# Kernel optimization log

Measured on AMD Instinct MI355X. Metric: run time of the kernel, lower is better.

Reference implementation:

```python
import jax, jax.numpy as jnp
import numpy as np

B, L, D_MODEL, HEADS = 4, 2048, 1024, 16
D_K = D_MODEL // HEADS
EPS = 1e-8
ROPE_BASE = 10000.0


def setup_inputs() -> dict:
    key = jax.random.key(0)
    k1, k2, k3 = jax.random.split(key, 3)
    x = jax.random.normal(k1, (B, L, D_MODEL), jnp.float32)
    W_in = jax.random.normal(k2, (3 * D_MODEL, D_MODEL), jnp.float32) * 0.02
    W_o = jax.random.normal(k3, (D_MODEL, D_MODEL), jnp.float32) * 0.02
    return {"x": x, "W_in": W_in, "W_o": W_o}


def _layer_norm(x, eps=EPS):
    # F.layer_norm with no affine params
    mu = jnp.mean(x, axis=-1, keepdims=True)
    var = jnp.var(x, axis=-1, keepdims=True)
    return (x - mu) * jax.lax.rsqrt(var + eps)


def _rope(x):
    # x: [B, H, L, d_k]; interleaved-pair rotary embedding
    seq = x.shape[2]
    half = x.shape[-1] // 2
    inv_freq = 1.0 / (ROPE_BASE ** (jnp.arange(half, dtype=jnp.float32) * 2.0 / x.shape[-1]))
    ang = jnp.arange(seq, dtype=jnp.float32)[:, None] * inv_freq[None, :]  # [L, half]
    cos, sin = jnp.cos(ang), jnp.sin(ang)
    x1, x2 = x[..., 0::2], x[..., 1::2]
    r1 = x1 * cos - x2 * sin
    r2 = x1 * sin + x2 * cos
    return jnp.stack([r1, r2], axis=-1).reshape(x.shape)


def reference(x, W_in, W_o):
    h = _layer_norm(x)
    qkv = h @ W_in.T  # [B, L, 3*D]
    q, k, v = jnp.split(qkv, 3, axis=-1)
    to_heads = lambda t: t.reshape(B, L, HEADS, D_K).transpose(0, 2, 1, 3)  # [B,H,L,dk]
    q, k, v = to_heads(q), to_heads(k), to_heads(v)
    q, k = _rope(q), _rope(k)
    scale = 1.0 / np.sqrt(D_K).astype(np.float32)
    scores = jnp.einsum('bhqd,bhkd->bhqk', q, k) * scale
    causal = jnp.tril(jnp.ones((L, L), dtype=bool))
    scores = jnp.where(causal, scores, -jnp.inf)
    attn = jax.nn.softmax(scores, axis=-1)
    o = jnp.einsum('bhqk,bhkd->bhqd', attn, v)
    o = o.transpose(0, 2, 1, 3).reshape(B, L, D_MODEL)
    return o @ W_o.T
```

## Files before the change

### kernel.cpp

```cpp
#include <hip/hip_runtime.h>
#include <cstdint>

typedef unsigned short u16;
typedef short bf16x8 __attribute__((ext_vector_type(8)));
typedef float f32x4 __attribute__((ext_vector_type(4)));
typedef float f32x16 __attribute__((ext_vector_type(16)));
typedef unsigned int u32x2 __attribute__((ext_vector_type(2)));
typedef unsigned int u32x4 __attribute__((ext_vector_type(4)));

#define NB 4
#define SEQ 2048
#define DMODEL 1024
#define NHEADS 16
#define DHEAD 64
#define BHTOT (NB*NHEADS)
#define MROWS (NB*SEQ)

__device__ __forceinline__ float bf2f(u16 u){
  union { unsigned int i; float f; } x; x.i = ((unsigned int)u)<<16; return x.f;
}
__device__ __forceinline__ u16 f2bf(float f){
  union { float f; unsigned int i; } x; x.f = f;
  unsigned int r = x.i + 0x7fffu + ((x.i>>16)&1u);
  return (u16)(r>>16);
}
__device__ __forceinline__ float fexp2(float x){
#if __has_builtin(__builtin_amdgcn_exp2f)
  return __builtin_amdgcn_exp2f(x);
#else
  return exp2f(x);
#endif
}

typedef const __attribute__((address_space(1))) unsigned int* gas_t;
typedef __attribute__((address_space(3))) unsigned int* las_t;
__device__ __forceinline__ void async_cp16(const void* g, void* l){
  __builtin_amdgcn_global_load_lds((gas_t)g, (las_t)l, 16, 0, 0);
}

__device__ __forceinline__ void plswap(unsigned int &a, unsigned int &b){
#if __has_builtin(__builtin_amdgcn_permlane32_swap)
  u32x2 r = __builtin_amdgcn_permlane32_swap(a, b, false, false);
  a = r[0]; b = r[1];
#else
  asm("v_permlane32_swap_b32 %0, %1" : "+v"(a), "+v"(b));
#endif
}

__global__ __launch_bounds__(256) void cast2_kernel(const float* __restrict__ wa, u16* __restrict__ oa,
    const float* __restrict__ wb, u16* __restrict__ ob, int na4){
  int i = blockIdx.x*256 + threadIdx.x;
  const float* src; u16* dst; int j;
  if(i < na4){ src = wa; dst = oa; j = i; }
  else       { src = wb; dst = ob; j = i - na4; }
  float4 v = ((const float4*)src)[j];
  ushort4 o;
  o.x=f2bf(v.x); o.y=f2bf(v.y); o.z=f2bf(v.z); o.w=f2bf(v.w);
  ((ushort4*)dst)[j] = o;
}

__global__ __launch_bounds__(256) void ln_kernel(const float* __restrict__ x, u16* __restrict__ h){
  int row = blockIdx.x;
  const float* xr = x + (size_t)row*DMODEL;
  u16* hr = h + (size_t)row*DMODEL;
  int t = threadIdx.x;
  float4 v = ((const float4*)xr)[t];
  float f0=v.x, f1=v.y, f2=v.z, f3=v.w;
  float s = f0+f1+f2+f3;
  float q = f0*f0+f1*f1+f2*f2+f3*f3;
  #pragma unroll
  for(int off=32; off; off>>=1){ s += __shfl_xor(s, off); q += __shfl_xor(q, off); }
  __shared__ float ss[4], sq[4];
  int wv = t>>6, lane = t&63;
  if(lane==0){ ss[wv]=s; sq[wv]=q; }
  __syncthreads();
  s = ss[0]+ss[1]+ss[2]+ss[3];
  q = sq[0]+sq[1]+sq[2]+sq[3];
  float mu  = s * (1.0f/DMODEL);
  float var = q * (1.0f/DMODEL) - mu*mu;
  float rs  = rsqrtf(var + 1e-8f);
  ushort4 o;
  o.x=f2bf((f0-mu)*rs); o.y=f2bf((f1-mu)*rs); o.z=f2bf((f2-mu)*rs); o.w=f2bf((f3-mu)*rs);
  ((ushort4*)hr)[t] = o;
}

#define BM 128
#define BN 128
#define BK 32

template<int MODE>
__global__ __launch_bounds__(256) void gemm_bt(const u16* __restrict__ A, const u16* __restrict__ Bm,
    u16* __restrict__ Qb, u16* __restrict__ Kb, u16* __restrict__ Vtb, float* __restrict__ outf,
    int M, int N, int K){
  __shared__ u16 As[2][BM*BK];
  __shared__ u16 Bs[2][BN*BK];
  int t = threadIdx.x;
  int lane = t&63, wv = t>>6;
  int c = lane&15, g = lane>>4;
  int wm = wv>>1, wn = wv&1;
  int m0 = blockIdx.y*BM, n0 = blockIdx.x*BN;

  int p0 = t>>3,        j0 = t&7;        int js0 = j0 ^ (p0&7);
  int p1 = (t+256)>>3,  j1 = t&7;        int js1 = j1 ^ (p1&7);
  size_t aoff0 = (size_t)(p0*2 + (js0>>2))*K + (js0&3)*8;
  size_t aoff1 = (size_t)(p1*2 + (js1>>2))*K + (js1&3)*8;
  const u16* Abase = A  + (size_t)m0*K;
  const u16* Bbase = Bm + (size_t)n0*K;

  f32x4 acc[4][4] = {};

  async_cp16(Abase + aoff0, &As[0][t*8]);
  async_cp16(Abase + aoff1, &As[0][(t+256)*8]);
  async_cp16(Bbase + aoff0, &Bs[0][t*8]);
  async_cp16(Bbase + aoff1, &Bs[0][(t+256)*8]);

  int cur = 0;
  for(int k0=0;k0<K;k0+=BK){
    __syncthreads();
    if(k0+BK < K){
      int nb = cur^1;
      async_cp16(Abase + (k0+BK) + aoff0, &As[nb][t*8]);
      async_cp16(Abase + (k0+BK) + aoff1, &As[nb][(t+256)*8]);
      async_cp16(Bbase + (k0+BK) + aoff0, &Bs[nb][t*8]);
      async_cp16(Bbase + (k0+BK) + aoff1, &Bs[nb][(t+256)*8]);
    }
    bf16x8 af[4], bfr[4];
    #pragma unroll
    for(int i=0;i<4;i++){
      int ra = wm*64 + i*16 + c;
      int qa = ((ra&1)*4 + g) ^ ((ra>>1)&7);
      af[i]  = *(const bf16x8*)(&As[cur][(ra>>1)*64 + qa*8]);
      int rb = wn*64 + i*16 + c;
      int qb = ((rb&1)*4 + g) ^ ((rb>>1)&7);
      bfr[i] = *(const bf16x8*)(&Bs[cur][(rb>>1)*64 + qb*8]);
    }
    #pragma unroll
    for(int mi=0;mi<4;mi++)
      #pragma unroll
      for(int ni=0;ni<4;ni++)
        acc[mi][ni] = __builtin_amdgcn_mfma_f32_16x16x32_bf16(af[mi], bfr[ni], acc[mi][ni], 0,0,0);
    cur ^= 1;
  }
  if(MODE==1){
    #pragma unroll
    for(int mi=0;mi<4;mi++){
      int mrow = m0 + wm*64 + mi*16 + g*4;
      #pragma unroll
      for(int ni=0;ni<4;ni++){
        int ncol = n0 + wn*64 + ni*16 + c;
        #pragma unroll
        for(int r=0;r<4;r++)
          outf[(size_t)(mrow+r)*N + ncol] = acc[mi][ni][r];
      }
    }
  } else {
    #pragma unroll
    for(int ni=0;ni<4;ni++){
      int n = n0 + wn*64 + ni*16 + c;
      int sel = n>>10, head = (n>>6)&15, d = n&63;
      #pragma unroll
      for(int mi=0;mi<4;mi++){
        int m = m0 + wm*64 + mi*16 + g*4;
        int b = m>>11, l = m&(SEQ-1);
        if(sel<2){
          u16* dst = (sel==0?Qb:Kb) + ((size_t)((b*NHEADS+head)*SEQ + l))*DHEAD + d;
          #pragma unroll
          for(int r=0;r<4;r++) dst[(size_t)r*DHEAD] = f2bf(acc[mi][ni][r]);
        } else {
          ushort4 pk;
          pk.x=f2bf(acc[mi][ni][0]); pk.y=f2bf(acc[mi][ni][1]);
          pk.z=f2bf(acc[mi][ni][2]); pk.w=f2bf(acc[mi][ni][3]);
          *(ushort4*)(&Vtb[((size_t)((b*NHEADS+head)*DHEAD + d))*SEQ + l]) = pk;
        }
      }
    }
  }
}

#define SC2 0.180336879f
__global__ __launch_bounds__(256) void rope_kernel(u16* __restrict__ Q, u16* __restrict__ Kb){
  int tid = blockIdx.x*256 + threadIdx.x;
  int j = tid&31, l = tid>>5;
  float inv = exp2f(-(float)j * (13.28771237954945f/32.0f));
  float sn, cs;
  sincosf((float)l*inv, &sn, &cs);
  size_t base = (size_t)l*DHEAD + 2*j;
  #pragma unroll 4
  for(int bh=0; bh<BHTOT; bh++){
    size_t off = base + (size_t)bh*SEQ*DHEAD;
    ushort2 q2 = *(ushort2*)(&Q[off]);
    float x1=bf2f(q2.x), x2=bf2f(q2.y);
    ushort2 o;
    o.x = f2bf((x1*cs - x2*sn)*SC2); o.y = f2bf((x1*sn + x2*cs)*SC2);
    *(ushort2*)(&Q[off]) = o;
    ushort2 k2 = *(ushort2*)(&Kb[off]);
    x1=bf2f(k2.x); x2=bf2f(k2.y);
    o.x = f2bf(x1*cs - x2*sn); o.y = f2bf(x1*sn + x2*cs);
    *(ushort2*)(&Kb[off]) = o;
  }
}


#define QKS32(QF) { \
  f32x16 z_ = {}; \
  z_ = __builtin_amdgcn_mfma_f32_32x32x16_bf16(kf[0], QF[0], z_, 0,0,0); \
  z_ = __builtin_amdgcn_mfma_f32_32x32x16_bf16(kf[1], QF[1], z_, 0,0,0); \
  z_ = __builtin_amdgcn_mfma_f32_32x32x16_bf16(kf[2], QF[2], z_, 0,0,0); \
  z_ = __builtin_amdgcn_mfma_f32_32x32x16_bf16(kf[3], QF[3], z_, 0,0,0); \
  sc = z_; }

#define LDK { \
  _Pragma("unroll") for(int dk_=0;dk_<4;dk_++){ \
    int kb_ = (c32*128 + dk_*32 + hl*16) ^ ((c32&7)<<4); \
    kf[dk_] = *(const bf16x8*)((const char*)(&Kls[cur][0]) + kb_); } }

#define LDV { \
  _Pragma("unroll") for(int dt_=0;dt_<2;dt_++) \
    _Pragma("unroll") for(int ks_=0;ks_<2;ks_++){ \
      int d_ = dt_*32 + c32; \
      int vb_ = (d_*64 + ks_*32 + hl*16) ^ (((d_>>1)&7)<<4); \
      vf[dt_][ks_] = *(const bf16x8*)((const char*)(&Vls[cur][0]) + vb_); } }

#define EXPPACK(MASKED, LROW) { \
  unsigned int pk_[8]; \
  _Pragma("unroll") for(int j_=0;j_<8;j_++){ \
    float a_ = fexp2(sc[2*j_]); \
    float b_ = fexp2(sc[2*j_+1]); \
    if(MASKED){ \
      int k0_ = ((2*j_)&3)   + 8*((2*j_)>>2)   + 4*hl; \
      int k1_ = ((2*j_+1)&3) + 8*((2*j_+1)>>2) + 4*hl; \
      a_ = (k0_ <= c32) ? a_ : 0.f; \
      b_ = (k1_ <= c32) ? b_ : 0.f; } \
    LROW += a_ + b_; \
    asm("v_cvt_pk_bf16_f32 %0, %1, %2" : "=v"(pk_[j_]) : "v"(a_), "v"(b_)); } \
  plswap(pk_[0], pk_[2]); \
  plswap(pk_[1], pk_[3]); \
  plswap(pk_[4], pk_[6]); \
  plswap(pk_[5], pk_[7]); \
  u32x4 wa_ = { pk_[0], pk_[1], pk_[2], pk_[3] }; \
  u32x4 wb_ = { pk_[4], pk_[5], pk_[6], pk_[7] }; \
  pa0 = __builtin_bit_cast(bf16x8, wa_); \
  pa1 = __builtin_bit_cast(bf16x8, wb_); }

#define PVM32(O0, O1) { \
  O0 = __builtin_amdgcn_mfma_f32_32x32x16_bf16(pa0, vf[0][0], O0, 0,0,0); \
  O0 = __builtin_amdgcn_mfma_f32_32x32x16_bf16(pa1, vf[0][1], O0, 0,0,0); \
  O1 = __builtin_amdgcn_mfma_f32_32x32x16_bf16(pa0, vf[1][0], O1, 0,0,0); \
  O1 = __builtin_amdgcn_mfma_f32_32x32x16_bf16(pa1, vf[1][1], O1, 0,0,0); }

#define STAGE(TILE, BUF) { \
  u16* dst_ = isK ? &Kls[BUF][cch*8] : &Vls[BUF][cch*8]; \
  async_cp16(sbase + soff0 + (size_t)(TILE)*sstep, dst_); }

__global__ __launch_bounds__(512, 2) void attn_kernel(const u16* __restrict__ Q, const u16* __restrict__ Kb,
    const u16* __restrict__ Vt, u16* __restrict__ O){
  __shared__ u16 Kls[4][2048];
  __shared__ u16 Vls[4][2048];
  __shared__ float LsA[8][32];
  __shared__ float LsB[8][32];
  int t = threadIdx.x, lane = t&63, w = t>>6;
  int c32 = lane&31, hl = lane>>5, h8 = hl*8;
  int bh = blockIdx.x;
  int b = bh>>4, hh = bh&15;
  int y = blockIdx.y;
  int sA = 8*y + w;
  int sB = 63 - 8*y - w;
  int NT = 64 - 8*y;
  const u16* Qp = Q  + (size_t)bh*SEQ*DHEAD;
  const u16* Kp = Kb + (size_t)bh*SEQ*DHEAD;
  const u16* Vp = Vt + (size_t)bh*DHEAD*SEQ;

  bool isK = (w < 4);
  int cch = isK ? t : (t - 256);
  int prow = cch>>3;
  int jsrc = (cch&7) ^ (prow&7);
  size_t soff0, sstep;
  if(isK){
    soff0 = (size_t)prow*64 + (size_t)jsrc*8;
    sstep = 32*64;
  } else {
    int c2 = prow*8 + jsrc;
    soff0 = (size_t)(c2>>2)*SEQ + (size_t)(c2&3)*8;
    sstep = 32;
  }
  const u16* sbase = isK ? Kp : Vp;

  bf16x8 qfA[4], qfB[4];
  #pragma unroll
  for(int dk=0;dk<4;dk++){
    qfA[dk] = *(const bf16x8*)(&Qp[(size_t)(sA*32 + c32)*DHEAD + dk*16 + h8]);
    qfB[dk] = *(const bf16x8*)(&Qp[(size_t)(sB*32 + c32)*DHEAD + dk*16 + h8]);
  }

  f32x16 oaccA0 = {}, oaccA1 = {}, oaccB0 = {}, oaccB1 = {};
  float lrowA = 0.f, lrowB = 0.f;
  f32x16 sc;
  bf16x8 kf[4], vf[2][2], pa0, pa1;

  STAGE(0, 0);
  STAGE(1, 1);
  STAGE(2, 2);

  #pragma unroll 1
  for(int tt=0; tt<NT; ++tt){
    asm volatile("s_waitcnt vmcnt(2)" ::: "memory");
    asm volatile("s_barrier" ::: "memory");
    if(tt+3 < NT){ STAGE(tt+3, (tt+3)&3); }
    int cur = tt&3;
    if(tt <= sB){
      LDK; LDV;
      QKS32(qfB);
      if(tt == sB){ EXPPACK(1, lrowB); } else { EXPPACK(0, lrowB); }
      PVM32(oaccB0, oaccB1);
      if(tt <= sA){
        QKS32(qfA);
        if(tt == sA){ EXPPACK(1, lrowA); } else { EXPPACK(0, lrowA); }
        PVM32(oaccA0, oaccA1);
      }
    }
  }

  float lrA = lrowA + __shfl_xor(lrowA, 32);
  float lrB = lrowB + __shfl_xor(lrowB, 32);
  __syncthreads();
  if(hl==0){ LsA[w][c32] = lrA; LsB[w][c32] = lrB; }
  __syncthreads();
  #pragma unroll
  for(int r=0;r<16;r++){
    int row = (r&3)+8*(r>>2)+4*hl;
    float livA = 1.0f/LsA[w][row];
    float livB = 1.0f/LsB[w][row];
    size_t oA = ((size_t)(b*SEQ + sA*32 + row))*DMODEL + hh*DHEAD;
    size_t oB = ((size_t)(b*SEQ + sB*32 + row))*DMODEL + hh*DHEAD;
    O[oA + c32]      = f2bf(oaccA0[r]*livA);
    O[oA + 32 + c32] = f2bf(oaccA1[r]*livA);
    O[oB + c32]      = f2bf(oaccB0[r]*livB);
    O[oB + 32 + c32] = f2bf(oaccB1[r]*livB);
  }
}

extern "C" void kernel_launch(void* const* d_in, const int* in_sizes, int n_in,
                              void* d_out, int out_size, void* d_ws, size_t ws_size,
                              hipStream_t stream){
  const float* x    = (const float*)d_in[0];
  const float* W_in = (const float*)d_in[1];
  const float* W_o  = (const float*)d_in[2];
  u16* ws = (u16*)d_ws;
  const size_t T16 = (size_t)8*1024*1024;
  u16* h   = ws;
  u16* Qb  = ws +   T16;
  u16* Kb  = ws + 2*T16;
  u16* Vtb = ws + 3*T16;
  u16* Wb  = ws + 4*T16;
  u16* Wob = Wb + (size_t)3*DMODEL*DMODEL;
  u16* Ob  = h;
  float* out = (float*)d_out;

  const int na4 = 3*DMODEL*DMODEL/4;
  const int nb4 = DMODEL*DMODEL/4;
  cast2_kernel<<<dim3((na4+nb4)/256), dim3(256), 0, stream>>>(W_in, Wb, W_o, Wob, na4);
  ln_kernel<<<dim3(MROWS), dim3(256), 0, stream>>>(x, h);
  gemm_bt<0><<<dim3(3*DMODEL/BN, MROWS/BM), dim3(256), 0, stream>>>(
      h, Wb, Qb, Kb, Vtb, nullptr, MROWS, 3*DMODEL, DMODEL);
  rope_kernel<<<dim3(SEQ*32/256), dim3(256), 0, stream>>>(Qb, Kb);
  attn_kernel<<<dim3(BHTOT, 4), dim3(512), 0, stream>>>(Qb, Kb, Vtb, Ob);
  gemm_bt<1><<<dim3(DMODEL/BN, MROWS/BM), dim3(256), 0, stream>>>(
      Ob, Wob, nullptr, nullptr, nullptr, out, MROWS, DMODEL, DMODEL);
}
```

Measured before the change: 259.6 us.

## Widen GEMM tile to 128x256 with 8 waves and 4-stage async pipeline

The bf16 GEMM now uses a 128x256 block tile computed by 8 waves (512 threads) instead of 128x128 with 4 waves. The LDS double buffer becomes a 4-buffer ring with 3 tiles in flight, using explicit vmcnt waits and raw barriers instead of __syncthreads. The goal is more reuse of each A tile and better hiding of global-load latency. In exchange, LDS use rises to 96 KB per block and the output GEMM grid shrinks to 256 blocks, which may leave fewer blocks than compute units to fill.

```diff
diff --git a/kernel.cpp b/kernel.cpp
--- a/kernel.cpp
+++ b/kernel.cpp
@@ -85,62 +85,66 @@
 }
 
 #define BM 128
-#define BN 128
+#define BN 256
 #define BK 32
 
 template<int MODE>
-__global__ __launch_bounds__(256) void gemm_bt(const u16* __restrict__ A, const u16* __restrict__ Bm,
+__global__ __launch_bounds__(512, 2) void gemm_bt(const u16* __restrict__ A, const u16* __restrict__ Bm,
     u16* __restrict__ Qb, u16* __restrict__ Kb, u16* __restrict__ Vtb, float* __restrict__ outf,
     int M, int N, int K){
-  __shared__ u16 As[2][BM*BK];
-  __shared__ u16 Bs[2][BN*BK];
+  __shared__ u16 As[4][BM*BK];
+  __shared__ u16 Bs[4][BN*BK];
   int t = threadIdx.x;
   int lane = t&63, wv = t>>6;
   int c = lane&15, g = lane>>4;
-  int wm = wv>>1, wn = wv&1;
+  int wm = wv>>2, wn = wv&3;
   int m0 = blockIdx.y*BM, n0 = blockIdx.x*BN;
 
-  int p0 = t>>3,        j0 = t&7;        int js0 = j0 ^ (p0&7);
-  int p1 = (t+256)>>3,  j1 = t&7;        int js1 = j1 ^ (p1&7);
-  size_t aoff0 = (size_t)(p0*2 + (js0>>2))*K + (js0&3)*8;
-  size_t aoff1 = (size_t)(p1*2 + (js1>>2))*K + (js1&3)*8;
+  int pA = t>>3, jA = t&7; int jsA = jA ^ (pA&7);
+  size_t aoff = (size_t)(pA*2 + (jsA>>2))*K + (jsA&3)*8;
   const u16* Abase = A  + (size_t)m0*K;
   const u16* Bbase = Bm + (size_t)n0*K;
 
+#define GSTAGE(TILE, BUF) { \
+    size_t k_ = (size_t)(TILE)*BK; \
+    async_cp16(Abase + k_ + aoff,            &As[BUF][t*8]); \
+    async_cp16(Bbase + k_ + aoff,            &Bs[BUF][t*8]); \
+    async_cp16(Bbase + k_ + aoff + 128*(size_t)K, &Bs[BUF][(t+512)*8]); }
+
   f32x4 acc[4][4] = {};
-
-  async_cp16(Abase + aoff0, &As[0][t*8]);
-  async_cp16(Abase + aoff1, &As[0][(t+256)*8]);
-  async_cp16(Bbase + aoff0, &Bs[0][t*8]);
-  async_cp16(Bbase + aoff1, &Bs[0][(t+256)*8]);
-
-  int cur = 0;
-  for(int k0=0;k0<K;k0+=BK){
-    __syncthreads();
-    if(k0+BK < K){
-      int nb = cur^1;
-      async_cp16(Abase + (k0+BK) + aoff0, &As[nb][t*8]);
-      async_cp16(Abase + (k0+BK) + aoff1, &As[nb][(t+256)*8]);
-      async_cp16(Bbase + (k0+BK) + aoff0, &Bs[nb][t*8]);
-      async_cp16(Bbase + (k0+BK) + aoff1, &Bs[nb][(t+256)*8]);
-    }
+  int NK = K/BK;
+
+  GSTAGE(0, 0);
+  GSTAGE(1, 1);
+  GSTAGE(2, 2);
+
+  #pragma unroll 1
+  for(int tt=0; tt<NK; ++tt){
+    if(tt < NK-2)      { asm volatile("s_waitcnt vmcnt(6)" ::: "memory"); }
+    else if(tt == NK-2){ asm volatile("s_waitcnt vmcnt(3)" ::: "memory"); }
+    else               { asm volatile("s_waitcnt vmcnt(0)" ::: "memory"); }
+    asm volatile("s_barrier" ::: "memory");
+    if(tt+3 < NK){ GSTAGE(tt+3, (tt+3)&3); }
+    const u16* As_ = As[tt&3];
+    const u16* Bs_ = Bs[tt&3];
     bf16x8 af[4], bfr[4];
     #pragma unroll
     for(int i=0;i<4;i++){
       int ra = wm*64 + i*16 + c;
       int qa = ((ra&1)*4 + g) ^ ((ra>>1)&7);
-      af[i]  = *(const bf16x8*)(&As[cur][(ra>>1)*64 + qa*8]);
+      af[i]  = *(const bf16x8*)(&As_[(ra>>1)*64 + qa*8]);
       int rb = wn*64 + i*16 + c;
       int qb = ((rb&1)*4 + g) ^ ((rb>>1)&7);
-      bfr[i] = *(const bf16x8*)(&Bs[cur][(rb>>1)*64 + qb*8]);
+      bfr[i] = *(const bf16x8*)(&Bs_[(rb>>1)*64 + qb*8]);
     }
     #pragma unroll
     for(int mi=0;mi<4;mi++)
       #pragma unroll
       for(int ni=0;ni<4;ni++)
         acc[mi][ni] = __builtin_amdgcn_mfma_f32_16x16x32_bf16(af[mi], bfr[ni], acc[mi][ni], 0,0,0);
-    cur ^= 1;
-  }
+  }
+#undef GSTAGE
+
   if(MODE==1){
     #pragma unroll
     for(int mi=0;mi<4;mi++){
@@ -360,10 +364,10 @@
   const int nb4 = DMODEL*DMODEL/4;
   cast2_kernel<<<dim3((na4+nb4)/256), dim3(256), 0, stream>>>(W_in, Wb, W_o, Wob, na4);
   ln_kernel<<<dim3(MROWS), dim3(256), 0, stream>>>(x, h);
-  gemm_bt<0><<<dim3(3*DMODEL/BN, MROWS/BM), dim3(256), 0, stream>>>(
+  gemm_bt<0><<<dim3(3*DMODEL/BN, MROWS/BM), dim3(512), 0, stream>>>(
       h, Wb, Qb, Kb, Vtb, nullptr, MROWS, 3*DMODEL, DMODEL);
   rope_kernel<<<dim3(SEQ*32/256), dim3(256), 0, stream>>>(Qb, Kb);
   attn_kernel<<<dim3(BHTOT, 4), dim3(512), 0, stream>>>(Qb, Kb, Vtb, Ob);
-  gemm_bt<1><<<dim3(DMODEL/BN, MROWS/BM), dim3(256), 0, stream>>>(
+  gemm_bt<1><<<dim3(DMODEL/BN, MROWS/BM), dim3(512), 0, stream>>>(
       Ob, Wob, nullptr, nullptr, nullptr, out, MROWS, DMODEL, DMODEL);
 }
```

New measurement: 283.8 us. 1.09x slower.
